# Performance work log

Measured on AMD Instinct MI355X. Metric: run time of the kernel, lower is better.

The kernel has to match this reference:

```python
import jax, jax.numpy as jnp
import numpy as np

COS_EPS = 1e-6   # torch CosineSimilarity eps
NORM_EPS = 1e-10 # assignment-normalizer eps


def setup_inputs() -> dict:
    key = jax.random.key(0)
    ks = jax.random.split(key, 12)
    s = 0.1
    H, K, Din, Dout = 8, 128, 64, 64
    return {
        "node_set": jax.random.normal(ks[0], (32, Din, 1024, 12), jnp.float32),
        "adj": jax.random.uniform(ks[1], (32, 1024, 1024), jnp.float32),
        "W0": jax.random.normal(ks[2], (Din, Din), jnp.float32) * s,
        "w_i2c": jax.random.normal(ks[3], (H, 1), jnp.float32) * s,
        "b_i2c": jax.random.normal(ks[4], (H,), jnp.float32) * s,
        "W_lin": jax.random.normal(ks[5], (H * K, H), jnp.float32) * s,
        "b_lin": jax.random.normal(ks[6], (H * K,), jnp.float32) * s,
        "conv_w": jax.random.normal(ks[7], (H,), jnp.float32) * s,
        "conv_b": jax.random.normal(ks[8], (), jnp.float32) * s,
        "W_feat": jax.random.normal(ks[9], (Dout, Din), jnp.float32) * s,
        "b_feat": jax.random.normal(ks[10], (Dout,), jnp.float32) * s,
    }


def reference(node_set, adj, W0, w_i2c, b_i2c, W_lin, b_lin, conv_w, conv_b, W_feat, b_feat):
    # [B, C, N, T] -> [B, N, C, T] -> mean over T -> [B, N, D]
    x = jnp.mean(jnp.transpose(node_set, (0, 2, 1, 3)), axis=3)
    B = x.shape[0]
    H = w_i2c.shape[0]
    K = W_lin.shape[0] // H

    # get_att: attention-pooled global centroid seed [B, 1, D]
    temp = jnp.mean(x, axis=1, keepdims=True)                 # [B,1,D]
    h_avg = jnp.tanh(jnp.einsum('bod,de->boe', temp, W0))    # [B,1,D]
    att = jnp.einsum('bnd,bod->bno', x, h_avg)               # [B,N,1]
    cent = jnp.einsum('bno,bnd->bod', att, x)                # [B,1,D]

    # generate batch centroids: [B,D,1] -> [B,D,H] -> [B,D,H*K] -> [B,H,K,D]
    bc = jnp.transpose(cent, (0, 2, 1))                       # [B,D,1]
    bc = jax.nn.relu(bc @ w_i2c.T + b_i2c)                    # [B,D,H]
    bc = jax.nn.relu(bc @ W_lin.T + b_lin)                    # [B,D,H*K]
    bc = jnp.transpose(bc, (0, 2, 1)).reshape(B, H, K, -1)    # [B,H,K,D]

    # cosine-similarity assignment (no 5D repeat: dot / max(|x||c|, eps))
    dots = jnp.einsum('bnd,bhkd->bhkn', x, bc)                # [B,H,K,N]
    xn = jnp.linalg.norm(x, axis=-1)                          # [B,N]
    cn = jnp.linalg.norm(bc, axis=-1)                         # [B,H,K]
    C_heads = dots / jnp.maximum(cn[..., None] * xn[:, None, None, :], COS_EPS)
    # normalize over centroids dim (dim 2)
    C_heads = C_heads / (jnp.sum(C_heads, axis=2, keepdims=True) + NORM_EPS)

    # 1x1 conv over heads -> single assignment matrix [B,K,N]
    C = jnp.einsum('h,bhkn->bkn', conv_w, C_heads) + conv_b

    # pooled node features + output projection
    new_node_set = jnp.einsum('bkn,bnd->bkd', C, x)           # [B,K,D]
    return new_node_set @ W_feat.T + b_feat                   # [B,K,Dout]
```

## Files before the change

kernel.cpp:

```cpp
#include <hip/hip_runtime.h>
#include <math.h>

#define B_  32
#define N_  1024
#define D_  64
#define H_  8
#define K_  128
#define HK_ 1024

__global__ __launch_bounds__(512) void k1_mean(const float* __restrict__ ns,
        float* __restrict__ x, float* __restrict__ invxn,
        float* __restrict__ tempsum) {
    __shared__ float tile[64][65];
    int b    = blockIdx.x >> 4;
    int n0   = (blockIdx.x & 15) << 6;
    int lane = threadIdx.x & 63;
    int w    = threadIdx.x >> 6;
    #pragma unroll
    for (int j = 0; j < 8; ++j) {
        int d = w * 8 + j;
        const float4* p = (const float4*)(ns +
            ((size_t)((b * 64 + d) * 1024 + n0 + lane)) * 12);
        float4 a = p[0], c = p[1], e = p[2];
        float s = ((a.x + a.y) + (a.z + a.w)) + ((c.x + c.y) + (c.z + c.w))
                + ((e.x + e.y) + (e.z + e.w));
        tile[lane][d] = s * (1.0f / 12.0f);
    }
    __syncthreads();
    #pragma unroll
    for (int j = 0; j < 8; ++j) {
        int r = w * 8 + j;
        float v = tile[r][lane];
        x[((size_t)(b * 1024 + n0 + r)) * 64 + lane] = v;
        float ss = v * v;
        #pragma unroll
        for (int o = 32; o; o >>= 1) ss += __shfl_xor(ss, o);
        if (lane == 0) invxn[b * 1024 + n0 + r] = 1.0f / sqrtf(fmaxf(ss, 1e-30f));
    }
    if (threadIdx.x < 64) {
        float s = 0.0f;
        #pragma unroll 16
        for (int r = 0; r < 64; ++r) s += tile[r][threadIdx.x];
        atomicAdd(&tempsum[b * 64 + threadIdx.x], s);
    }
}

__global__ __launch_bounds__(256) void k3_cent(const float* __restrict__ x,
        const float* __restrict__ tempsum, const float* __restrict__ W0,
        float* __restrict__ cent) {
    __shared__ float t[64];
    __shared__ float ha[64];
    __shared__ float cp[4][64];
    int b    = blockIdx.x >> 4;
    int n0   = (blockIdx.x & 15) << 6;
    int lane = threadIdx.x & 63;
    int w    = threadIdx.x >> 6;
    if (threadIdx.x < 64) t[threadIdx.x] = tempsum[b * 64 + threadIdx.x] * (1.0f / 1024.0f);
    __syncthreads();
    if (threadIdx.x < 64) {
        float a = 0.0f;
        #pragma unroll 8
        for (int d = 0; d < 64; ++d) a += t[d] * W0[d * 64 + threadIdx.x];
        ha[threadIdx.x] = tanhf(a);
    }
    __syncthreads();
    float hv = ha[lane];
    float cw = 0.0f;
    for (int nn = w; nn < 64; nn += 4) {
        float xv = x[((size_t)(b * 1024 + n0 + nn)) * 64 + lane];
        float d  = xv * hv;
        #pragma unroll
        for (int o = 32; o; o >>= 1) d += __shfl_xor(d, o);
        cw += d * xv;
    }
    cp[w][lane] = cw;
    __syncthreads();
    if (w == 0)
        atomicAdd(&cent[b * 64 + lane],
                  cp[0][lane] + cp[1][lane] + cp[2][lane] + cp[3][lane]);
}

__global__ __launch_bounds__(256) void k4_bc(const float* __restrict__ cent,
        const float* __restrict__ w_i2c, const float* __restrict__ b_i2c,
        const float* __restrict__ W_lin, const float* __restrict__ b_lin,
        float* __restrict__ bc, float* __restrict__ invcn) {
    int lane = threadIdx.x & 63;
    int w    = threadIdx.x >> 6;
    int gg   = blockIdx.x * 4 + w;
    int b    = gg >> 8;
    int kk0  = (gg & 255) * 4;
    float c = cent[b * 64 + lane];
    float b1[8];
    #pragma unroll
    for (int h = 0; h < 8; ++h) b1[h] = fmaxf(c * w_i2c[h] + b_i2c[h], 0.0f);
    #pragma unroll
    for (int u = 0; u < 4; ++u) {
        int kk = kk0 + u;
        float pre = b_lin[kk];
        #pragma unroll
        for (int h = 0; h < 8; ++h) pre += b1[h] * W_lin[kk * 8 + h];
        float v = fmaxf(pre, 0.0f);
        bc[((size_t)(b * 1024 + kk)) * 64 + lane] = v;
        float ss = v * v;
        #pragma unroll
        for (int o = 32; o; o >>= 1) ss += __shfl_xor(ss, o);
        if (lane == 0) invcn[b * 1024 + kk] = (ss > 0.0f) ? (1.0f / sqrtf(ss)) : 0.0f;
    }
}

__global__ __launch_bounds__(256, 2) void k5_assign(const float* __restrict__ x,
        const float* __restrict__ bc, const float* __restrict__ invxn,
        const float* __restrict__ invcn, const float* __restrict__ conv_w,
        const float* __restrict__ conv_b, float* __restrict__ C) {
    __shared__ float xt[64][68];
    __shared__ float bct[128][68];
    __shared__ float invx_s[64];
    __shared__ float invc_s[128];
    __shared__ float sred[16][68];
    __shared__ float sinv[64];
    int b   = blockIdx.x >> 4;
    int n0  = (blockIdx.x & 15) << 6;
    int tid = threadIdx.x;
    {
        int r = tid >> 2, dh = (tid & 3) << 4;
        const float4* src = (const float4*)(x + ((size_t)(b * 1024 + n0 + r)) * 64 + dh);
        float4* dst = (float4*)(&xt[r][dh]);
        dst[0] = src[0]; dst[1] = src[1]; dst[2] = src[2]; dst[3] = src[3];
    }
    if (tid < 64) invx_s[tid] = invxn[b * 1024 + n0 + tid];
    float Cacc[8][4];
    #pragma unroll
    for (int i = 0; i < 8; ++i)
        #pragma unroll
        for (int j = 0; j < 4; ++j) Cacc[i][j] = 0.0f;
    int q = tid >> 4, p = tid & 15;
    float cb = conv_b[0];
    for (int h = 0; h < 8; ++h) {
        {
            int r = tid >> 1, dh = (tid & 1) << 5;
            const float4* src = (const float4*)(bc + ((size_t)(b * 1024 + h * 128 + r)) * 64 + dh);
            float4* dst = (float4*)(&bct[r][dh]);
            #pragma unroll
            for (int u = 0; u < 8; ++u) dst[u] = src[u];
        }
        if (tid < 128) invc_s[tid] = invcn[b * 1024 + h * 128 + tid];
        __syncthreads();
        float acc[8][4];
        #pragma unroll
        for (int i = 0; i < 8; ++i)
            #pragma unroll
            for (int j = 0; j < 4; ++j) acc[i][j] = 0.0f;
        for (int dc = 0; dc < 64; dc += 4) {
            float4 bv[8], xv[4];
            #pragma unroll
            for (int i = 0; i < 8; ++i) bv[i] = *(const float4*)(&bct[q + 16 * i][dc]);
            #pragma unroll
            for (int j = 0; j < 4; ++j) xv[j] = *(const float4*)(&xt[p + 16 * j][dc]);
            #pragma unroll
            for (int i = 0; i < 8; ++i)
                #pragma unroll
                for (int j = 0; j < 4; ++j)
                    acc[i][j] += bv[i].x * xv[j].x + bv[i].y * xv[j].y
                               + bv[i].z * xv[j].z + bv[i].w * xv[j].w;
        }
        float part[4];
        #pragma unroll
        for (int j = 0; j < 4; ++j) part[j] = 0.0f;
        #pragma unroll
        for (int i = 0; i < 8; ++i) {
            float ic = invc_s[q + 16 * i];
            #pragma unroll
            for (int j = 0; j < 4; ++j) {
                float v = acc[i][j] * ic * invx_s[p + 16 * j];
                acc[i][j] = v;
                part[j] += v;
            }
        }
        #pragma unroll
        for (int j = 0; j < 4; ++j) sred[q][p + 16 * j] = part[j];
        __syncthreads();
        if (tid < 64) {
            float s = 0.0f;
            #pragma unroll
            for (int qq = 0; qq < 16; ++qq) s += sred[qq][tid];
            sinv[tid] = 1.0f / (s + 1e-10f);
        }
        __syncthreads();
        float cwv = conv_w[h];
        #pragma unroll
        for (int j = 0; j < 4; ++j) {
            float si = sinv[p + 16 * j];
            #pragma unroll
            for (int i = 0; i < 8; ++i) Cacc[i][j] += cwv * acc[i][j] * si;
        }
        __syncthreads();
    }
    #pragma unroll
    for (int i = 0; i < 8; ++i) {
        int k = q + 16 * i;
        #pragma unroll
        for (int j = 0; j < 4; ++j)
            C[((size_t)(b * 128 + k)) * 1024 + n0 + p + 16 * j] = Cacc[i][j] + cb;
    }
}

__global__ __launch_bounds__(256, 2) void k6_out(const float* __restrict__ C,
        const float* __restrict__ x, const float* __restrict__ Wf,
        const float* __restrict__ bfeat, float* __restrict__ out) {
    __shared__ float xt[128][68];
    __shared__ float ct[16][132];
    __shared__ float nnst[16][68];
    __shared__ float wfs[64][68];
    int b   = blockIdx.x >> 3;
    int k0  = (blockIdx.x & 7) << 4;
    int tid = threadIdx.x;
    int kq  = tid >> 4, p = tid & 15;
    for (int t = tid; t < 4096; t += 256) wfs[t >> 6][t & 63] = Wf[t];
    float acc[4] = {0.0f, 0.0f, 0.0f, 0.0f};
    for (int c = 0; c < 8; ++c) {
        __syncthreads();
        {
            int r = tid >> 1, dh = (tid & 1) << 5;
            const float4* src = (const float4*)(x + ((size_t)(b * 1024 + c * 128 + r)) * 64 + dh);
            float4* dst = (float4*)(&xt[r][dh]);
            #pragma unroll
            for (int u = 0; u < 8; ++u) dst[u] = src[u];
        }
        for (int t = tid; t < 2048; t += 256)
            ct[t >> 7][t & 127] = C[((size_t)(b * 128 + k0 + (t >> 7))) * 1024 + c * 128 + (t & 127)];
        __syncthreads();
        #pragma unroll 8
        for (int n = 0; n < 128; ++n) {
            float  cv = ct[kq][n];
            float4 xv = *(const float4*)(&xt[n][p << 2]);
            acc[0] += cv * xv.x; acc[1] += cv * xv.y;
            acc[2] += cv * xv.z; acc[3] += cv * xv.w;
        }
    }
    __syncthreads();
    nnst[kq][(p << 2) + 0] = acc[0];
    nnst[kq][(p << 2) + 1] = acc[1];
    nnst[kq][(p << 2) + 2] = acc[2];
    nnst[kq][(p << 2) + 3] = acc[3];
    __syncthreads();
    float o0 = bfeat[(p << 2) + 0], o1 = bfeat[(p << 2) + 1];
    float o2 = bfeat[(p << 2) + 2], o3 = bfeat[(p << 2) + 3];
    #pragma unroll
    for (int dc = 0; dc < 64; dc += 4) {
        float4 nv = *(const float4*)(&nnst[kq][dc]);
        float4 w0 = *(const float4*)(&wfs[(p << 2) + 0][dc]);
        float4 w1 = *(const float4*)(&wfs[(p << 2) + 1][dc]);
        float4 w2 = *(const float4*)(&wfs[(p << 2) + 2][dc]);
        float4 w3 = *(const float4*)(&wfs[(p << 2) + 3][dc]);
        o0 += nv.x * w0.x + nv.y * w0.y + nv.z * w0.z + nv.w * w0.w;
        o1 += nv.x * w1.x + nv.y * w1.y + nv.z * w1.z + nv.w * w1.w;
        o2 += nv.x * w2.x + nv.y * w2.y + nv.z * w2.z + nv.w * w2.w;
        o3 += nv.x * w3.x + nv.y * w3.y + nv.z * w3.z + nv.w * w3.w;
    }
    float4 ov = make_float4(o0, o1, o2, o3);
    *(float4*)(out + ((size_t)(b * 128 + k0 + kq)) * 64 + (p << 2)) = ov;
}

extern "C" void kernel_launch(void* const* d_in, const int* in_sizes, int n_in,
                              void* d_out, int out_size, void* d_ws, size_t ws_size,
                              hipStream_t stream) {
    const float* node_set = (const float*)d_in[0];
    const float* W0     = (const float*)d_in[2];
    const float* w_i2c  = (const float*)d_in[3];
    const float* b_i2c  = (const float*)d_in[4];
    const float* W_lin  = (const float*)d_in[5];
    const float* b_lin  = (const float*)d_in[6];
    const float* conv_w = (const float*)d_in[7];
    const float* conv_b = (const float*)d_in[8];
    const float* W_feat = (const float*)d_in[9];
    const float* b_feat = (const float*)d_in[10];
    float* out = (float*)d_out;
    float* ws  = (float*)d_ws;

    float* x       = ws;
    float* invxn   = ws + 2097152;
    float* tempsum = ws + 2129920;
    float* cent    = ws + 2131968;
    float* bc      = ws + 2134016;
    float* invcn   = ws + 4231168;
    float* Cmat    = ws + 4263936;

    hipMemsetAsync(tempsum, 0, 4096 * sizeof(float), stream);

    k1_mean  <<<B_ * 16, 512, 0, stream>>>(node_set, x, invxn, tempsum);
    k3_cent  <<<B_ * 16, 256, 0, stream>>>(x, tempsum, W0, cent);
    k4_bc    <<<2048,    256, 0, stream>>>(cent, w_i2c, b_i2c, W_lin, b_lin, bc, invcn);
    k5_assign<<<B_ * 16, 256, 0, stream>>>(x, bc, invxn, invcn, conv_w, conv_b, Cmat);
    k6_out   <<<B_ * 8,  256, 0, stream>>>(Cmat, x, W_feat, b_feat, out);
}
```

Before: 379.4 us.

## Replace atomics with partial-sum buffers and prefetch next head in assign kernel

The global atomic reductions for the temporal mean sum and the centroid are replaced by per-block partial buffers. Consumer kernels sum these buffers, which removes the memset launch and makes the reduction deterministic. The centroid kernel now uses fewer blocks, each covering more nodes. In the assignment kernel, the next head's centroid tile is loaded into registers while the current head computes, and the per-column normaliser is computed redundantly per thread instead of through an extra shared buffer. This removes two barriers per head at the cost of more registers and fewer blocks in k3.

```diff
diff --git a/kernel.cpp b/kernel.cpp
--- a/kernel.cpp
+++ b/kernel.cpp
@@ -10,7 +10,7 @@
 
 __global__ __launch_bounds__(512) void k1_mean(const float* __restrict__ ns,
         float* __restrict__ x, float* __restrict__ invxn,
-        float* __restrict__ tempsum) {
+        float* __restrict__ part1) {
     __shared__ float tile[64][65];
     int b    = blockIdx.x >> 4;
     int n0   = (blockIdx.x & 15) << 6;
@@ -41,21 +41,26 @@
         float s = 0.0f;
         #pragma unroll 16
         for (int r = 0; r < 64; ++r) s += tile[r][threadIdx.x];
-        atomicAdd(&tempsum[b * 64 + threadIdx.x], s);
+        part1[(size_t)blockIdx.x * 64 + threadIdx.x] = s;
     }
 }
 
 __global__ __launch_bounds__(256) void k3_cent(const float* __restrict__ x,
-        const float* __restrict__ tempsum, const float* __restrict__ W0,
-        float* __restrict__ cent) {
+        const float* __restrict__ part1, const float* __restrict__ W0,
+        float* __restrict__ part2) {
     __shared__ float t[64];
     __shared__ float ha[64];
     __shared__ float cp[4][64];
-    int b    = blockIdx.x >> 4;
-    int n0   = (blockIdx.x & 15) << 6;
+    int b    = blockIdx.x >> 2;
+    int n0   = (blockIdx.x & 3) << 8;
     int lane = threadIdx.x & 63;
     int w    = threadIdx.x >> 6;
-    if (threadIdx.x < 64) t[threadIdx.x] = tempsum[b * 64 + threadIdx.x] * (1.0f / 1024.0f);
+    if (threadIdx.x < 64) {
+        float s = 0.0f;
+        #pragma unroll
+        for (int j = 0; j < 16; ++j) s += part1[(size_t)(b * 16 + j) * 64 + threadIdx.x];
+        t[threadIdx.x] = s * (1.0f / 1024.0f);
+    }
     __syncthreads();
     if (threadIdx.x < 64) {
         float a = 0.0f;
@@ -66,7 +71,7 @@
     __syncthreads();
     float hv = ha[lane];
     float cw = 0.0f;
-    for (int nn = w; nn < 64; nn += 4) {
+    for (int nn = w; nn < 256; nn += 4) {
         float xv = x[((size_t)(b * 1024 + n0 + nn)) * 64 + lane];
         float d  = xv * hv;
         #pragma unroll
@@ -76,11 +81,11 @@
     cp[w][lane] = cw;
     __syncthreads();
     if (w == 0)
-        atomicAdd(&cent[b * 64 + lane],
-                  cp[0][lane] + cp[1][lane] + cp[2][lane] + cp[3][lane]);
-}
-
-__global__ __launch_bounds__(256) void k4_bc(const float* __restrict__ cent,
+        part2[(size_t)blockIdx.x * 64 + lane] =
+            ((cp[0][lane] + cp[1][lane]) + (cp[2][lane] + cp[3][lane]));
+}
+
+__global__ __launch_bounds__(256) void k4_bc(const float* __restrict__ part2,
         const float* __restrict__ w_i2c, const float* __restrict__ b_i2c,
         const float* __restrict__ W_lin, const float* __restrict__ b_lin,
         float* __restrict__ bc, float* __restrict__ invcn) {
@@ -89,7 +94,9 @@
     int gg   = blockIdx.x * 4 + w;
     int b    = gg >> 8;
     int kk0  = (gg & 255) * 4;
-    float c = cent[b * 64 + lane];
+    float c = 0.0f;
+    #pragma unroll
+    for (int s = 0; s < 4; ++s) c += part2[(size_t)(b * 4 + s) * 64 + lane];
     float b1[8];
     #pragma unroll
     for (int h = 0; h < 8; ++h) b1[h] = fmaxf(c * w_i2c[h] + b_i2c[h], 0.0f);
@@ -117,7 +124,6 @@
     __shared__ float invx_s[64];
     __shared__ float invc_s[128];
     __shared__ float sred[16][68];
-    __shared__ float sinv[64];
     int b   = blockIdx.x >> 4;
     int n0  = (blockIdx.x & 15) << 6;
     int tid = threadIdx.x;
@@ -128,6 +134,14 @@
         dst[0] = src[0]; dst[1] = src[1]; dst[2] = src[2]; dst[3] = src[3];
     }
     if (tid < 64) invx_s[tid] = invxn[b * 1024 + n0 + tid];
+    {
+        int r = tid >> 1, dh = (tid & 1) << 5;
+        const float4* src = (const float4*)(bc + ((size_t)(b * 1024 + r)) * 64 + dh);
+        float4* dst = (float4*)(&bct[r][dh]);
+        #pragma unroll
+        for (int u = 0; u < 8; ++u) dst[u] = src[u];
+    }
+    if (tid < 128) invc_s[tid] = invcn[b * 1024 + tid];
     float Cacc[8][4];
     #pragma unroll
     for (int i = 0; i < 8; ++i)
@@ -135,16 +149,18 @@
         for (int j = 0; j < 4; ++j) Cacc[i][j] = 0.0f;
     int q = tid >> 4, p = tid & 15;
     float cb = conv_b[0];
+    int rr = tid >> 1, dhh = (tid & 1) << 5;
     for (int h = 0; h < 8; ++h) {
+        __syncthreads();
+        int hn = (h + 1) & 7;
+        float4 pf[8];
+        float  pfc = 0.0f;
         {
-            int r = tid >> 1, dh = (tid & 1) << 5;
-            const float4* src = (const float4*)(bc + ((size_t)(b * 1024 + h * 128 + r)) * 64 + dh);
-            float4* dst = (float4*)(&bct[r][dh]);
-            #pragma unroll
-            for (int u = 0; u < 8; ++u) dst[u] = src[u];
-        }
-        if (tid < 128) invc_s[tid] = invcn[b * 1024 + h * 128 + tid];
-        __syncthreads();
+            const float4* src = (const float4*)(bc + ((size_t)(b * 1024 + hn * 128 + rr)) * 64 + dhh);
+            #pragma unroll
+            for (int u = 0; u < 8; ++u) pf[u] = src[u];
+        }
+        if (tid < 128) pfc = invcn[b * 1024 + hn * 128 + tid];
         float acc[8][4];
         #pragma unroll
         for (int i = 0; i < 8; ++i)
@@ -179,21 +195,22 @@
         #pragma unroll
         for (int j = 0; j < 4; ++j) sred[q][p + 16 * j] = part[j];
         __syncthreads();
-        if (tid < 64) {
+        {
+            float4* dst = (float4*)(&bct[rr][dhh]);
+            #pragma unroll
+            for (int u = 0; u < 8; ++u) dst[u] = pf[u];
+        }
+        if (tid < 128) invc_s[tid] = pfc;
+        float cwv = conv_w[h];
+        #pragma unroll
+        for (int j = 0; j < 4; ++j) {
             float s = 0.0f;
             #pragma unroll
-            for (int qq = 0; qq < 16; ++qq) s += sred[qq][tid];
-            sinv[tid] = 1.0f / (s + 1e-10f);
-        }
-        __syncthreads();
-        float cwv = conv_w[h];
-        #pragma unroll
-        for (int j = 0; j < 4; ++j) {
-            float si = sinv[p + 16 * j];
+            for (int qq = 0; qq < 16; ++qq) s += sred[qq][p + 16 * j];
+            float si = 1.0f / (s + 1e-10f);
             #pragma unroll
             for (int i = 0; i < 8; ++i) Cacc[i][j] += cwv * acc[i][j] * si;
         }
-        __syncthreads();
     }
     #pragma unroll
     for (int i = 0; i < 8; ++i) {
@@ -277,19 +294,17 @@
     float* out = (float*)d_out;
     float* ws  = (float*)d_ws;
 
-    float* x       = ws;
-    float* invxn   = ws + 2097152;
-    float* tempsum = ws + 2129920;
-    float* cent    = ws + 2131968;
-    float* bc      = ws + 2134016;
-    float* invcn   = ws + 4231168;
-    float* Cmat    = ws + 4263936;
-
-    hipMemsetAsync(tempsum, 0, 4096 * sizeof(float), stream);
-
-    k1_mean  <<<B_ * 16, 512, 0, stream>>>(node_set, x, invxn, tempsum);
-    k3_cent  <<<B_ * 16, 256, 0, stream>>>(x, tempsum, W0, cent);
-    k4_bc    <<<2048,    256, 0, stream>>>(cent, w_i2c, b_i2c, W_lin, b_lin, bc, invcn);
+    float* x     = ws;
+    float* invxn = ws + 2097152;
+    float* part1 = ws + 2129920;
+    float* part2 = ws + 2162688;
+    float* bc    = ws + 2170880;
+    float* invcn = ws + 4268032;
+    float* Cmat  = ws + 4300800;
+
+    k1_mean  <<<B_ * 16, 512, 0, stream>>>(node_set, x, invxn, part1);
+    k3_cent  <<<B_ * 4,  256, 0, stream>>>(x, part1, W0, part2);
+    k4_bc    <<<2048,    256, 0, stream>>>(part2, w_i2c, b_i2c, W_lin, b_lin, bc, invcn);
     k5_assign<<<B_ * 16, 256, 0, stream>>>(x, bc, invxn, invcn, conv_w, conv_b, Cmat);
     k6_out   <<<B_ * 8,  256, 0, stream>>>(Cmat, x, W_feat, b_feat, out);
 }
```

Measured after the change: 419.1 us. +10.5%, slower.
